# Kernel optimization log

Measured on AMD Instinct MI355X. Metric: run time of the kernel, lower is better.

The kernel has to match this reference:

```python
import jax, jax.numpy as jnp
import numpy as np

HIGH_THRESHOLD = 0.1
EPS = 1e-6


def _gaussian_kernel_2d(ksize=5, sigma=1.0):
    x = np.arange(ksize, dtype=np.float32) - ksize // 2
    g = np.exp(-(x * x) / (2.0 * sigma * sigma))
    g = g / g.sum()
    return (g[:, None] * g[None, :]).astype(np.float32)  # (5,5)


def _sobel_kernels():
    gx = np.array([[-1.0, 0.0, 1.0], [-2.0, 0.0, 2.0], [-1.0, 0.0, 1.0]], np.float32)
    gy = gx.T.copy()
    return np.stack([gx, gy])[:, None]  # (2,1,3,3)


def _nms_kernels():
    # kornia get_canny_nms_kernel: 8 direction kernels, center 1, -1 at neighbor
    k = np.zeros((8, 1, 3, 3), np.float32)
    k[:, 0, 1, 1] = 1.0
    offs = [(1, 2), (0, 2), (0, 1), (0, 0), (1, 0), (2, 0), (2, 1), (2, 2)]
    for i, (r, c) in enumerate(offs):
        k[i, 0, r, c] = -1.0
    return k


def _conv(x, w, pad, mode=None):
    # x: (B,Cin,H,W), w: (Cout,Cin,kh,kw)
    if mode is not None:
        x = jnp.pad(x, ((0, 0), (0, 0), (pad, pad), (pad, pad)), mode=mode)
        padding = 'VALID'
    else:
        padding = [(pad, pad), (pad, pad)]
    return jax.lax.conv_general_dilated(
        x, w, (1, 1), padding, dimension_numbers=('NCHW', 'OIHW', 'NCHW'))


def cal_edge(x):
    dt = x.dtype
    if x.shape[1] == 3:  # rgb_to_grayscale
        w = jnp.array([0.299, 0.587, 0.114], dt).reshape(1, 3, 1, 1)
        x = jnp.sum(x * w, axis=1, keepdims=True)
    # gaussian_blur2d, reflect border (kornia default)
    blurred = _conv(x, jnp.asarray(_gaussian_kernel_2d())[None, None], 2, mode='reflect')
    # spatial_gradient (sobel, replicate border)
    grads = _conv(blurred, jnp.asarray(_sobel_kernels()), 1, mode='edge')  # (B,2,H,W)
    gx, gy = grads[:, 0:1], grads[:, 1:2]
    magnitude = jnp.sqrt(gx * gx + gy * gy + EPS)  # (B,1,H,W)
    angle = jnp.arctan2(gy, gx) * (180.0 / np.pi)
    angle = jnp.round(angle / 45.0) * 45.0
    nms_mag = _conv(magnitude, jnp.asarray(_nms_kernels()), 1)  # (B,8,H,W), zero pad
    pos_idx = jnp.mod(angle / 45.0, 8.0).astype(jnp.int32)        # (B,1,H,W)
    neg_idx = jnp.mod(angle / 45.0 + 4.0, 8.0).astype(jnp.int32)
    cp = jnp.take_along_axis(nms_mag, pos_idx, axis=1)
    cn = jnp.take_along_axis(nms_mag, neg_idx, axis=1)
    is_max = jnp.minimum(cp, cn) > 0.0
    magnitude = magnitude * is_max
    # F.threshold(mag, high, 0); then F.threshold(-e, -high, -1); e = -e
    e1 = jnp.where(magnitude > HIGH_THRESHOLD, magnitude, jnp.zeros((), dt))
    edges = -jnp.where(-e1 > -HIGH_THRESHOLD, -e1, jnp.full((), -1.0, dt))
    return edges


def setup_inputs() -> dict:
    key = jax.random.key(0)
    k1, k2 = jax.random.split(key)
    shape = (8, 3, 1024, 1024)
    op = jax.random.uniform(k1, shape, jnp.float32)
    gt = jax.random.uniform(k2, shape, jnp.float32)
    return {'op': op, 'gt': gt}


def reference(op, gt):
    edge_op = cal_edge(op)
    edge_gt = cal_edge(gt)
    return jnp.mean(jnp.abs(edge_op - edge_gt))
```

## Files before the change

### kernel.cpp

```cpp
#include <hip/hip_runtime.h>

#define N 1024
#define NN (N * N)
#define STRIPS 19
#define SEGS 64
#define SEGROWS 16
#define NUNITS (STRIPS * SEGS * 8)

__device__ __forceinline__ int refl(int i) {
    if (i < 0) return -i;
    if (i >= N) return 2 * N - 2 - i;
    return i;
}

#define ROW_BODY(yv, DO_NMS)                                                      \
  {                                                                               \
    int rr = ROWE ? refl(yv) : (yv);                                              \
    const float* ra = A + (size_t)rr * N;      \
    const float* rb = B + (size_t)rr * N;                                         \
    float ga = 0.299f * ra[cR] + 0.587f * ra[cR + NN] + 0.114f * ra[cR + 2 * NN]; \
    float gb = 0.299f * rb[cR] + 0.587f * rb[cR + NN] + 0.114f * rb[cR + 2 * NN]; \
    float gal2 = __shfl(ga, iL2, 64), gal1 = __shfl(ga, iL1, 64);                 \
    float gar1 = __shfl(ga, iR1, 64), gar2 = __shfl(ga, iR2, 64);                 \
    float gbl2 = __shfl(gb, iL2, 64), gbl1 = __shfl(gb, iL1, 64);                 \
    float gbr1 = __shfl(gb, iR1, 64), gbr2 = __shfl(gb, iR2, 64);                 \
    float hna = w0*gal2 + w1*gal1 + w2*ga + w3*gar1 + w4*gar2;                    \
    float hnb = w0*gbl2 + w1*gbl1 + w2*gb + w3*gbr1 + w4*gbr2;                    \
    ha0=ha1; ha1=ha2; ha2=ha3; ha3=ha4; ha4=hna;                                  \
    hb0=hb1; hb1=hb2; hb2=hb3; hb3=hb4; hb4=hnb;                                  \
    float bna = w0*ha0 + w1*ha1 + w2*ha2 + w3*ha3 + w4*ha4;                       \
    float bnb = w0*hb0 + w1*hb1 + w2*hb2 + w3*hb3 + w4*hb4;                       \
    bla0=bla1; bla1=bla2; bla2=bna;                                               \
    blb0=blb1; blb1=blb2; blb2=bnb;                                               \
    float Ara, Cra, Arb, Crb;                                                     \
    if (ROWE) {                                                                   \
      int z = (yv) - 3;                                                           \
      Ara = (z == 0)     ? bla1 : bla0;                                           \
      Cra = (z == N - 1) ? bla1 : bla2;                                           \
      Arb = (z == 0)     ? blb1 : blb0;                                           \
      Crb = (z == N - 1) ? blb1 : blb2;                                           \
    } else { Ara = bla0; Cra = bla2; Arb = blb0; Crb = blb2; }                    \
    float sa = Ara + 2.f*bla1 + Cra;  float da = Cra - Ara;                       \
    float sb = Arb + 2.f*blb1 + Crb;  float db = Crb - Arb;                       \
    float sal = __shfl(sa, iL1, 64), sar = __shfl(sa, iR1, 64);                   \
    float dal = __shfl(da, iL1, 64), dar = __shfl(da, iR1, 64);                   \
    float sbl = __shfl(sb, iL1, 64), sbr = __shfl(sb, iR1, 64);                   \
    float dbl = __shfl(db, iL1, 64), dbr = __shfl(db, iR1, 64);                   \
    if (COLE) {                                                                   \
      sal = cz0 ? sa : sal;  dal = cz0 ? da : dal;                                \
      sar = czN ? sa : sar;  dar = czN ? da : dar;                                \
      sbl = cz0 ? sb : sbl;  dbl = cz0 ? db : dbl;                                \
      sbr = czN ? sb : sbr;  dbr = czN ? db : dbr;                                \
    }                                                                             \
    float gxa = sar - sal;            float gya = dal + 2.f*da + dar;             \
    float gxb = sbr - sbl;            float gyb = dbl + 2.f*db + dbr;             \
    float maga = sqrtf(gxa*gxa + gya*gya + 1e-6f);                                \
    float magb = sqrtf(gxb*gxb + gyb*gyb + 1e-6f);                                \
    float axx = fabsf(gxa), ayy = fabsf(gya);                                     \
    int cda = (ayy <= 0.41421356f * axx) ? 0                                      \
            : (ayy >= 2.41421356f * axx) ? 1                                      \
            : (((gxa > 0.f) == (gya > 0.f)) ? 2 : 3);                             \
    float bxx = fabsf(gxb), byy = fabsf(gyb);                                     \
    int cdb = (byy <= 0.41421356f * bxx) ? 0                                      \
            : (byy >= 2.41421356f * bxx) ? 1                                      \
            : (((gxb > 0.f) == (gyb > 0.f)) ? 2 : 3);                             \
    float mala = __shfl(maga, iL1, 64); if (COLE) mala = cz0 ? 0.f : mala;        \
    float mara = __shfl(maga, iR1, 64); if (COLE) mara = czN ? 0.f : mara;        \
    float malb = __shfl(magb, iL1, 64); if (COLE) malb = cz0 ? 0.f : malb;        \
    float marb = __shfl(magb, iR1, 64); if (COLE) marb = czN ? 0.f : marb;        \
    mga0=mga1;   mga1=mga2;   mga2=maga;                                          \
    mgla0=mgla1; mgla1=mgla2; mgla2=mala;                                         \
    mgra0=mgra1; mgra1=mgra2; mgra2=mara;                                         \
    mgb0=mgb1;   mgb1=mgb2;   mgb2=magb;                                          \
    mglb0=mglb1; mglb1=mglb2; mglb2=malb;                                         \
    mgrb0=mgrb1; mgrb1=mgrb2; mgrb2=marb;                                         \
    int axUa = axa; axa = cda;                                                    \
    int axUb = axb; axb = cdb;                                                    \
    if (DO_NMS) {                                                                 \
      float m0a = mga0, l0a = mgla0, r0a = mgra0;                                 \
      float m2a = mga2, l2a = mgla2, r2a = mgra2;                                 \
      float m0b = mgb0, l0b = mglb0, r0b = mgrb0;                                 \
      float m2b = mgb2, l2b = mglb2, r2b = mgrb2;                                 \
      if (ROWE) {                                                                 \
        int w = (yv) - 4;                                                         \
        if (w == 0)     { m0a=0; l0a=0; r0a=0; m0b=0; l0b=0; r0b=0; }             \
        if (w == N - 1) { m2a=0; l2a=0; r2a=0; m2b=0; l2b=0; r2b=0; }             \
      }                                                                           \
      float n1a = (axUa == 0) ? mgra1 : (axUa == 1) ? m0a : (axUa == 2) ? r0a : l0a; \
      float n2a = (axUa == 0) ? mgla1 : (axUa == 1) ? m2a : (axUa == 2) ? l2a : r2a; \
      float n1b = (axUb == 0) ? mgrb1 : (axUb == 1) ? m0b : (axUb == 2) ? r0b : l0b; \
      float n2b = (axUb == 0) ? mglb1 : (axUb == 1) ? m2b : (axUb == 2) ? l2b : r2b; \
      bool ea = (mga1 > n1a) && (mga1 > n2a) && (mga1 > 0.1f);                    \
      bool eb = (mgb1 > n1b) && (mgb1 > n2b) && (mgb1 > 0.1f);                    \
      acc += (int)(valid && (ea != eb));                                          \
    }                                                                             \
  }

template<bool COLE, bool ROWE>
__device__ __forceinline__ void edge_unit(
    const float* __restrict__ op, const float* __restrict__ gt,
    unsigned int* __restrict__ partials,
    int unit, int img, int strip, int seg, int lane)
{
    const float w0 = 0.05448868f, w1 = 0.24420134f, w2 = 0.40261996f,
                w3 = 0.24420134f, w4 = 0.05448868f;

    int cb = strip * 56 - 4;
    int c  = cb + lane;
    int cR = COLE ? refl(c) : c;

    const float* A = op + (size_t)img * 3 * NN;
    const float* B = gt + (size_t)img * 3 * NN;

    const bool cz0 = COLE && (c == 0);
    const bool czN = COLE && (c == N - 1);
    const bool valid = (lane >= 4) && (lane <= 59) &&
                       (!COLE || ((c >= 0) && (c < N)));

    const int iL1 = lane - 1, iL2 = lane - 2, iR1 = lane + 1, iR2 = lane + 2;

    float ha0=0,ha1=0,ha2=0,ha3=0,ha4=0;
    float bla0=0,bla1=0,bla2=0;
    float mga0=0,mga1=0,mga2=0;
    float mgla0=0,mgla1=0,mgla2=0;
    float mgra0=0,mgra1=0,mgra2=0;
    int   axa = 0;
    float hb0=0,hb1=0,hb2=0,hb3=0,hb4=0;
    float blb0=0,blb1=0,blb2=0;
    float mgb0=0,mgb1=0,mgb2=0;
    float mglb0=0,mglb1=0,mglb2=0;
    float mgrb0=0,mgrb1=0,mgrb2=0;
    int   axb = 0;

    int acc = 0;
    const int R0 = seg * SEGROWS;

#pragma unroll 4
    for (int y = R0 - 4; y < R0 + 4; ++y) ROW_BODY(y, 0)

#pragma unroll 4
    for (int y = R0 + 4; y <= R0 + SEGROWS + 3; ++y) ROW_BODY(y, 1)

    for (int off = 32; off > 0; off >>= 1)
        acc += __shfl_down(acc, off, 64);
    if (lane == 0)
        partials[unit] = (unsigned int)acc;
}

__global__ __launch_bounds__(256)
void edge_diff_kernel(const float* __restrict__ op, const float* __restrict__ gt,
                      unsigned int* __restrict__ partials)
{
    int lane = threadIdx.x & 63;
    int unit = blockIdx.x * 4 + (threadIdx.x >> 6);
    int img  = unit / (STRIPS * SEGS);
    int rem  = unit - img * (STRIPS * SEGS);
    int strip = rem >> 6;
    int seg   = rem & (SEGS - 1);

    bool cole = (strip == 0) || (strip == STRIPS - 1);
    bool rowe = (seg == 0)   || (seg == SEGS - 1);

    if (!cole) {
        if (!rowe) edge_unit<false, false>(op, gt, partials, unit, img, strip, seg, lane);
        else       edge_unit<false, true >(op, gt, partials, unit, img, strip, seg, lane);
    } else {
        if (!rowe) edge_unit<true,  false>(op, gt, partials, unit, img, strip, seg, lane);
        else       edge_unit<true,  true >(op, gt, partials, unit, img, strip, seg, lane);
    }
}

__global__ __launch_bounds__(256)
void finalize_kernel(const unsigned int* __restrict__ partials, float* __restrict__ out)
{
    __shared__ unsigned int ws[4];
    int tid = threadIdx.x;
    unsigned int sum = 0;
    for (int i = tid; i < NUNITS; i += 256)
        sum += partials[i];
    int d = (int)sum;
    for (int off = 32; off > 0; off >>= 1)
        d += __shfl_down(d, off, 64);
    if ((tid & 63) == 0) ws[tid >> 6] = (unsigned int)d;
    __syncthreads();
    if (tid == 0)
        out[0] = (float)(ws[0] + ws[1] + ws[2] + ws[3]) / 8388608.0f;
}

extern "C" void kernel_launch(void* const* d_in, const int* in_sizes, int n_in,
                              void* d_out, int out_size, void* d_ws, size_t ws_size,
                              hipStream_t stream)
{
    const float* op = (const float*)d_in[0];
    const float* gt = (const float*)d_in[1];
    unsigned int* partials = (unsigned int*)d_ws;

    edge_diff_kernel<<<dim3(NUNITS / 4), dim3(256), 0, stream>>>(op, gt, partials);
    finalize_kernel<<<1, dim3(256), 0, stream>>>(partials, (float*)d_out);
}
```

Measured before the change: 238.9 us.

## Process four columns per lane with float4 loads and register-prefetched rows

Each lane now handles four adjacent columns using float4 loads, so a wavefront covers 248 output columns instead of 56. This cuts the strip count from 19 to 5 and shrinks the halo redundancy and the number of cross-lane shuffles per pixel. Row data is prefetched two rows ahead into registers, and the non-maximum-suppression results are packed into bitmasks counted with popc. The row-edge warmup now runs the full pipeline stages. The cost is much higher register pressure from the four-wide state arrays, which may lower occupancy, and far fewer blocks are launched.

Result: slower. 360.6 us (+50.9%).

```diff
diff --git a/kernel.cpp b/kernel.cpp
--- a/kernel.cpp
+++ b/kernel.cpp
@@ -2,10 +2,11 @@
 
 #define N 1024
 #define NN (N * N)
-#define STRIPS 19
+#define STRIPS 5
 #define SEGS 64
 #define SEGROWS 16
 #define NUNITS (STRIPS * SEGS * 8)
+#define NBLOCKS (NUNITS / 4)
 
 __device__ __forceinline__ int refl(int i) {
     if (i < 0) return -i;
@@ -13,87 +14,139 @@
     return i;
 }
 
-#define ROW_BODY(yv, DO_NMS)                                                      \
-  {                                                                               \
-    int rr = ROWE ? refl(yv) : (yv);                                              \
-    const float* ra = A + (size_t)rr * N;      \
-    const float* rb = B + (size_t)rr * N;                                         \
-    float ga = 0.299f * ra[cR] + 0.587f * ra[cR + NN] + 0.114f * ra[cR + 2 * NN]; \
-    float gb = 0.299f * rb[cR] + 0.587f * rb[cR + NN] + 0.114f * rb[cR + 2 * NN]; \
-    float gal2 = __shfl(ga, iL2, 64), gal1 = __shfl(ga, iL1, 64);                 \
-    float gar1 = __shfl(ga, iR1, 64), gar2 = __shfl(ga, iR2, 64);                 \
-    float gbl2 = __shfl(gb, iL2, 64), gbl1 = __shfl(gb, iL1, 64);                 \
-    float gbr1 = __shfl(gb, iR1, 64), gbr2 = __shfl(gb, iR2, 64);                 \
-    float hna = w0*gal2 + w1*gal1 + w2*ga + w3*gar1 + w4*gar2;                    \
-    float hnb = w0*gbl2 + w1*gbl1 + w2*gb + w3*gbr1 + w4*gbr2;                    \
-    ha0=ha1; ha1=ha2; ha2=ha3; ha3=ha4; ha4=hna;                                  \
-    hb0=hb1; hb1=hb2; hb2=hb3; hb3=hb4; hb4=hnb;                                  \
-    float bna = w0*ha0 + w1*ha1 + w2*ha2 + w3*ha3 + w4*ha4;                       \
-    float bnb = w0*hb0 + w1*hb1 + w2*hb2 + w3*hb3 + w4*hb4;                       \
-    bla0=bla1; bla1=bla2; bla2=bna;                                               \
-    blb0=blb1; blb1=blb2; blb2=bnb;                                               \
-    float Ara, Cra, Arb, Crb;                                                     \
-    if (ROWE) {                                                                   \
-      int z = (yv) - 3;                                                           \
-      Ara = (z == 0)     ? bla1 : bla0;                                           \
-      Cra = (z == N - 1) ? bla1 : bla2;                                           \
-      Arb = (z == 0)     ? blb1 : blb0;                                           \
-      Crb = (z == N - 1) ? blb1 : blb2;                                           \
-    } else { Ara = bla0; Cra = bla2; Arb = blb0; Crb = blb2; }                    \
-    float sa = Ara + 2.f*bla1 + Cra;  float da = Cra - Ara;                       \
-    float sb = Arb + 2.f*blb1 + Crb;  float db = Crb - Arb;                       \
-    float sal = __shfl(sa, iL1, 64), sar = __shfl(sa, iR1, 64);                   \
-    float dal = __shfl(da, iL1, 64), dar = __shfl(da, iR1, 64);                   \
-    float sbl = __shfl(sb, iL1, 64), sbr = __shfl(sb, iR1, 64);                   \
-    float dbl = __shfl(db, iL1, 64), dbr = __shfl(db, iR1, 64);                   \
-    if (COLE) {                                                                   \
-      sal = cz0 ? sa : sal;  dal = cz0 ? da : dal;                                \
-      sar = czN ? sa : sar;  dar = czN ? da : dar;                                \
-      sbl = cz0 ? sb : sbl;  dbl = cz0 ? db : dbl;                                \
-      sbr = czN ? sb : sbr;  dbr = czN ? db : dbr;                                \
-    }                                                                             \
-    float gxa = sar - sal;            float gya = dal + 2.f*da + dar;             \
-    float gxb = sbr - sbl;            float gyb = dbl + 2.f*db + dbr;             \
-    float maga = sqrtf(gxa*gxa + gya*gya + 1e-6f);                                \
-    float magb = sqrtf(gxb*gxb + gyb*gyb + 1e-6f);                                \
-    float axx = fabsf(gxa), ayy = fabsf(gya);                                     \
-    int cda = (ayy <= 0.41421356f * axx) ? 0                                      \
-            : (ayy >= 2.41421356f * axx) ? 1                                      \
-            : (((gxa > 0.f) == (gya > 0.f)) ? 2 : 3);                             \
-    float bxx = fabsf(gxb), byy = fabsf(gyb);                                     \
-    int cdb = (byy <= 0.41421356f * bxx) ? 0                                      \
-            : (byy >= 2.41421356f * bxx) ? 1                                      \
-            : (((gxb > 0.f) == (gyb > 0.f)) ? 2 : 3);                             \
-    float mala = __shfl(maga, iL1, 64); if (COLE) mala = cz0 ? 0.f : mala;        \
-    float mara = __shfl(maga, iR1, 64); if (COLE) mara = czN ? 0.f : mara;        \
-    float malb = __shfl(magb, iL1, 64); if (COLE) malb = cz0 ? 0.f : malb;        \
-    float marb = __shfl(magb, iR1, 64); if (COLE) marb = czN ? 0.f : marb;        \
-    mga0=mga1;   mga1=mga2;   mga2=maga;                                          \
-    mgla0=mgla1; mgla1=mgla2; mgla2=mala;                                         \
-    mgra0=mgra1; mgra1=mgra2; mgra2=mara;                                         \
-    mgb0=mgb1;   mgb1=mgb2;   mgb2=magb;                                          \
-    mglb0=mglb1; mglb1=mglb2; mglb2=malb;                                         \
-    mgrb0=mgrb1; mgrb1=mgrb2; mgrb2=marb;                                         \
-    int axUa = axa; axa = cda;                                                    \
-    int axUb = axb; axb = cdb;                                                    \
-    if (DO_NMS) {                                                                 \
-      float m0a = mga0, l0a = mgla0, r0a = mgra0;                                 \
-      float m2a = mga2, l2a = mgla2, r2a = mgra2;                                 \
-      float m0b = mgb0, l0b = mglb0, r0b = mgrb0;                                 \
-      float m2b = mgb2, l2b = mglb2, r2b = mgrb2;                                 \
-      if (ROWE) {                                                                 \
-        int w = (yv) - 4;                                                         \
-        if (w == 0)     { m0a=0; l0a=0; r0a=0; m0b=0; l0b=0; r0b=0; }             \
-        if (w == N - 1) { m2a=0; l2a=0; r2a=0; m2b=0; l2b=0; r2b=0; }             \
-      }                                                                           \
-      float n1a = (axUa == 0) ? mgra1 : (axUa == 1) ? m0a : (axUa == 2) ? r0a : l0a; \
-      float n2a = (axUa == 0) ? mgla1 : (axUa == 1) ? m2a : (axUa == 2) ? l2a : r2a; \
-      float n1b = (axUb == 0) ? mgrb1 : (axUb == 1) ? m0b : (axUb == 2) ? r0b : l0b; \
-      float n2b = (axUb == 0) ? mglb1 : (axUb == 1) ? m2b : (axUb == 2) ? l2b : r2b; \
-      bool ea = (mga1 > n1a) && (mga1 > n2a) && (mga1 > 0.1f);                    \
-      bool eb = (mgb1 > n1b) && (mgb1 > n2b) && (mgb1 > 0.1f);                    \
-      acc += (int)(valid && (ea != eb));                                          \
-    }                                                                             \
+template<bool COLE, bool ROWE, int STAGE>
+static __device__ __forceinline__ int img_row(
+    int yv, float g0, float g1, float g2, float g3,
+    float (&h)[4][5], float (&bl)[4][3], float (&mg)[4][3],
+    float (&mL)[3], float (&mR)[3], int (&ax)[4], int (&axU)[4],
+    bool cz0, bool czN, int iL1, int iR1)
+{
+    const float w0 = 0.05448868f, w1 = 0.24420134f, w2 = 0.40261996f,
+                w3 = 0.24420134f, w4 = 0.05448868f;
+
+    float gm2 = __shfl(g2, iL1, 64), gm1 = __shfl(g3, iL1, 64);
+    float gp4 = __shfl(g0, iR1, 64), gp5 = __shfl(g1, iR1, 64);
+    float hn0 = w0*gm2 + w1*gm1 + w2*g0 + w3*g1 + w4*g2;
+    float hn1 = w0*gm1 + w1*g0 + w2*g1 + w3*g2 + w4*g3;
+    float hn2 = w0*g0  + w1*g1 + w2*g2 + w3*g3 + w4*gp4;
+    float hn3 = w0*g1  + w1*g2 + w2*g3 + w3*gp4 + w4*gp5;
+#pragma unroll
+    for (int j = 0; j < 4; ++j) {
+#pragma unroll
+        for (int k = 0; k < 4; ++k) h[j][k] = h[j][k+1];
+    }
+    h[0][4]=hn0; h[1][4]=hn1; h[2][4]=hn2; h[3][4]=hn3;
+    if (STAGE < 1) return 0;
+
+    float bn[4];
+#pragma unroll
+    for (int j = 0; j < 4; ++j)
+        bn[j] = w0*h[j][0] + w1*h[j][1] + w2*h[j][2] + w3*h[j][3] + w4*h[j][4];
+#pragma unroll
+    for (int j = 0; j < 4; ++j) { bl[j][0]=bl[j][1]; bl[j][1]=bl[j][2]; bl[j][2]=bn[j]; }
+    if (STAGE < 2) return 0;
+
+    float s[4], d[4];
+#pragma unroll
+    for (int j = 0; j < 4; ++j) {
+        float A_, C_;
+        if (ROWE) {
+            int z = yv - 3;
+            A_ = (z == 0)     ? bl[j][1] : bl[j][0];
+            C_ = (z == N - 1) ? bl[j][1] : bl[j][2];
+        } else { A_ = bl[j][0]; C_ = bl[j][2]; }
+        s[j] = A_ + 2.f*bl[j][1] + C_;
+        d[j] = C_ - A_;
+    }
+    float sL = __shfl(s[3], iL1, 64), dL = __shfl(d[3], iL1, 64);
+    float sR = __shfl(s[0], iR1, 64), dR = __shfl(d[0], iR1, 64);
+    if (COLE) {
+        sL = cz0 ? s[0] : sL;  dL = cz0 ? d[0] : dL;
+        sR = czN ? s[3] : sR;  dR = czN ? d[3] : dR;
+    }
+    float gx[4], gy[4];
+    gx[0] = s[1] - sL;   gy[0] = dL + 2.f*d[0] + d[1];
+    gx[1] = s[2] - s[0]; gy[1] = d[0] + 2.f*d[1] + d[2];
+    gx[2] = s[3] - s[1]; gy[2] = d[1] + 2.f*d[2] + d[3];
+    gx[3] = sR - s[2];   gy[3] = d[2] + 2.f*d[3] + dR;
+
+    float m[4]; int cd[4];
+#pragma unroll
+    for (int j = 0; j < 4; ++j) {
+        m[j] = sqrtf(gx[j]*gx[j] + gy[j]*gy[j] + 1e-6f);
+        float ax_ = fabsf(gx[j]), ay_ = fabsf(gy[j]);
+        cd[j] = (ay_ <= 0.41421356f * ax_) ? 0
+              : (ay_ >= 2.41421356f * ax_) ? 1
+              : (((gx[j] > 0.f) == (gy[j] > 0.f)) ? 2 : 3);
+    }
+    float mLn = __shfl(m[3], iL1, 64);
+    float mRn = __shfl(m[0], iR1, 64);
+    if (COLE) { mLn = cz0 ? 0.f : mLn;  mRn = czN ? 0.f : mRn; }
+#pragma unroll
+    for (int j = 0; j < 4; ++j) { mg[j][0]=mg[j][1]; mg[j][1]=mg[j][2]; mg[j][2]=m[j]; }
+    mL[0]=mL[1]; mL[1]=mL[2]; mL[2]=mLn;
+    mR[0]=mR[1]; mR[1]=mR[2]; mR[2]=mRn;
+#pragma unroll
+    for (int j = 0; j < 4; ++j) { axU[j] = ax[j]; ax[j] = cd[j]; }
+    if (STAGE < 3) return 0;
+
+    float rm1[6] = { mL[0], mg[0][0], mg[1][0], mg[2][0], mg[3][0], mR[0] };
+    float rc [6] = { mL[1], mg[0][1], mg[1][1], mg[2][1], mg[3][1], mR[1] };
+    float rp1[6] = { mL[2], mg[0][2], mg[1][2], mg[2][2], mg[3][2], mR[2] };
+    if (ROWE) {
+        int w = yv - 4;
+        if (w == 0) {
+#pragma unroll
+            for (int j = 0; j < 6; ++j) rm1[j] = 0.f;
+        }
+        if (w == N - 1) {
+#pragma unroll
+            for (int j = 0; j < 6; ++j) rp1[j] = 0.f;
+        }
+    }
+    int em = 0;
+#pragma unroll
+    for (int j = 1; j <= 4; ++j) {
+        int a_ = axU[j-1];
+        float n1 = (a_ == 0) ? rc[j+1] : (a_ == 1) ? rm1[j] : (a_ == 2) ? rm1[j+1] : rm1[j-1];
+        float n2 = (a_ == 0) ? rc[j-1] : (a_ == 1) ? rp1[j] : (a_ == 2) ? rp1[j-1] : rp1[j+1];
+        bool e = (rc[j] > n1) && (rc[j] > n2) && (rc[j] > 0.1f);
+        em |= (int)e << (j-1);
+    }
+    return em;
+}
+
+#define LOADROW(k, rrv) { size_t o_ = (size_t)(rrv) * N;                          \
+    if (!COLE) {                                                                  \
+      vAr##k = *(const float4*)(Ar + o_); vAg##k = *(const float4*)(Ag + o_);     \
+      vAb##k = *(const float4*)(Ab + o_);                                         \
+      vBr##k = *(const float4*)(Br + o_); vBg##k = *(const float4*)(Bg + o_);     \
+      vBb##k = *(const float4*)(Bb + o_);                                         \
+    } else {                                                                      \
+      vAr##k.x = Ar[o_+rq0]; vAr##k.y = Ar[o_+rq1]; vAr##k.z = Ar[o_+rq2]; vAr##k.w = Ar[o_+rq3]; \
+      vAg##k.x = Ag[o_+rq0]; vAg##k.y = Ag[o_+rq1]; vAg##k.z = Ag[o_+rq2]; vAg##k.w = Ag[o_+rq3]; \
+      vAb##k.x = Ab[o_+rq0]; vAb##k.y = Ab[o_+rq1]; vAb##k.z = Ab[o_+rq2]; vAb##k.w = Ab[o_+rq3]; \
+      vBr##k.x = Br[o_+rq0]; vBr##k.y = Br[o_+rq1]; vBr##k.z = Br[o_+rq2]; vBr##k.w = Br[o_+rq3]; \
+      vBg##k.x = Bg[o_+rq0]; vBg##k.y = Bg[o_+rq1]; vBg##k.z = Bg[o_+rq2]; vBg##k.w = Bg[o_+rq3]; \
+      vBb##k.x = Bb[o_+rq0]; vBb##k.y = Bb[o_+rq1]; vBb##k.z = Bb[o_+rq2]; vBb##k.w = Bb[o_+rq3]; \
+    } }
+
+#define BODY(yv, STAGE, kb, RELOAD) {                                             \
+    float ga0 = 0.299f*vAr##kb.x + 0.587f*vAg##kb.x + 0.114f*vAb##kb.x;           \
+    float ga1 = 0.299f*vAr##kb.y + 0.587f*vAg##kb.y + 0.114f*vAb##kb.y;           \
+    float ga2 = 0.299f*vAr##kb.z + 0.587f*vAg##kb.z + 0.114f*vAb##kb.z;           \
+    float ga3 = 0.299f*vAr##kb.w + 0.587f*vAg##kb.w + 0.114f*vAb##kb.w;           \
+    float gb0 = 0.299f*vBr##kb.x + 0.587f*vBg##kb.x + 0.114f*vBb##kb.x;           \
+    float gb1 = 0.299f*vBr##kb.y + 0.587f*vBg##kb.y + 0.114f*vBb##kb.y;           \
+    float gb2 = 0.299f*vBr##kb.z + 0.587f*vBg##kb.z + 0.114f*vBb##kb.z;           \
+    float gb3 = 0.299f*vBr##kb.w + 0.587f*vBg##kb.w + 0.114f*vBb##kb.w;           \
+    if (RELOAD) { int n_ = (yv) + 2; int r_ = ROWE ? refl(n_) : (n_);             \
+                  LOADROW(kb, r_) }                                               \
+    int emA = img_row<COLE,ROWE,STAGE>((yv), ga0,ga1,ga2,ga3,                     \
+                  ah,abl,amg,amL,amR,aax,aaxU, cz0,czN,iL1,iR1);                  \
+    int emB = img_row<COLE,ROWE,STAGE>((yv), gb0,gb1,gb2,gb3,                     \
+                  bh,bbl,bmg,bmL,bmR,bax,baxU, cz0,czN,iL1,iR1);                  \
+    if ((STAGE) >= 3) acc += valid ? __popc(emA ^ emB) : 0;                       \
   }
 
 template<bool COLE, bool ROWE>
@@ -102,44 +155,60 @@
     unsigned int* __restrict__ partials,
     int unit, int img, int strip, int seg, int lane)
 {
-    const float w0 = 0.05448868f, w1 = 0.24420134f, w2 = 0.40261996f,
-                w3 = 0.24420134f, w4 = 0.05448868f;
-
-    int cb = strip * 56 - 4;
-    int c  = cb + lane;
-    int cR = COLE ? refl(c) : c;
-
-    const float* A = op + (size_t)img * 3 * NN;
-    const float* B = gt + (size_t)img * 3 * NN;
-
-    const bool cz0 = COLE && (c == 0);
-    const bool czN = COLE && (c == N - 1);
-    const bool valid = (lane >= 4) && (lane <= 59) &&
-                       (!COLE || ((c >= 0) && (c < N)));
-
-    const int iL1 = lane - 1, iL2 = lane - 2, iR1 = lane + 1, iR2 = lane + 2;
-
-    float ha0=0,ha1=0,ha2=0,ha3=0,ha4=0;
-    float bla0=0,bla1=0,bla2=0;
-    float mga0=0,mga1=0,mga2=0;
-    float mgla0=0,mgla1=0,mgla2=0;
-    float mgra0=0,mgra1=0,mgra2=0;
-    int   axa = 0;
-    float hb0=0,hb1=0,hb2=0,hb3=0,hb4=0;
-    float blb0=0,blb1=0,blb2=0;
-    float mgb0=0,mgb1=0,mgb2=0;
-    float mglb0=0,mglb1=0,mglb2=0;
-    float mgrb0=0,mgrb1=0,mgrb2=0;
-    int   axb = 0;
+    const int cb = strip * 248 - 4;
+    const int c0 = cb + 4 * lane;
+
+    int rq0 = 0, rq1 = 0, rq2 = 0, rq3 = 0;
+    if (COLE) { rq0 = refl(c0); rq1 = refl(c0+1); rq2 = refl(c0+2); rq3 = refl(c0+3); }
+
+    const float* Ar = op + (size_t)img * 3 * NN + (COLE ? 0 : c0);
+    const float* Ag = Ar + NN;
+    const float* Ab = Ar + 2 * NN;
+    const float* Br = gt + (size_t)img * 3 * NN + (COLE ? 0 : c0);
+    const float* Bg = Br + NN;
+    const float* Bb = Br + 2 * NN;
+
+    const bool cz0 = COLE && (c0 == 0);
+    const bool czN = COLE && (c0 + 3 == N - 1);
+    const bool valid = (lane >= 1) && (lane <= 62) &&
+                       (!COLE || ((c0 >= 0) && (c0 + 3 < N)));
+
+    const int iL1 = lane - 1, iR1 = lane + 1;
+
+    float ah[4][5] = {}, bh[4][5] = {};
+    float abl[4][3] = {}, bbl[4][3] = {};
+    float amg[4][3] = {}, bmg[4][3] = {};
+    float amL[3] = {}, amR[3] = {}, bmL[3] = {}, bmR[3] = {};
+    int aax[4] = {}, aaxU[4] = {}, bax[4] = {}, baxU[4] = {};
+
+    float4 vAr0, vAg0, vAb0, vBr0, vBg0, vBb0;
+    float4 vAr1, vAg1, vAb1, vBr1, vBg1, vBb1;
 
     int acc = 0;
     const int R0 = seg * SEGROWS;
 
-#pragma unroll 4
-    for (int y = R0 - 4; y < R0 + 4; ++y) ROW_BODY(y, 0)
-
-#pragma unroll 4
-    for (int y = R0 + 4; y <= R0 + SEGROWS + 3; ++y) ROW_BODY(y, 1)
+    if (!ROWE) {
+        LOADROW(0, R0 - 4) LOADROW(1, R0 - 3)
+        BODY(R0 - 4, 0, 0, 1) BODY(R0 - 3, 0, 1, 1)
+        BODY(R0 - 2, 0, 0, 1) BODY(R0 - 1, 0, 1, 1)
+        BODY(R0,     1, 0, 1) BODY(R0 + 1, 1, 1, 1)
+        BODY(R0 + 2, 2, 0, 1) BODY(R0 + 3, 2, 1, 1)
+    } else {
+        LOADROW(0, refl(R0 - 4)) LOADROW(1, refl(R0 - 3))
+        BODY(R0 - 4, 2, 0, 1) BODY(R0 - 3, 2, 1, 1)
+        BODY(R0 - 2, 2, 0, 1) BODY(R0 - 1, 2, 1, 1)
+        BODY(R0,     2, 0, 1) BODY(R0 + 1, 2, 1, 1)
+        BODY(R0 + 2, 2, 0, 1) BODY(R0 + 3, 2, 1, 1)
+    }
+
+#pragma unroll 1
+    for (int t = 0; t < 7; ++t) {
+        int y = R0 + 4 + 2 * t;
+        BODY(y,     3, 0, 1)
+        BODY(y + 1, 3, 1, 1)
+    }
+    BODY(R0 + SEGROWS + 2, 3, 0, 0)
+    BODY(R0 + SEGROWS + 3, 3, 1, 0)
 
     for (int off = 32; off > 0; off >>= 1)
         acc += __shfl_down(acc, off, 64);
@@ -195,6 +264,6 @@
     const float* gt = (const float*)d_in[1];
     unsigned int* partials = (unsigned int*)d_ws;
 
-    edge_diff_kernel<<<dim3(NUNITS / 4), dim3(256), 0, stream>>>(op, gt, partials);
+    edge_diff_kernel<<<dim3(NBLOCKS), dim3(256), 0, stream>>>(op, gt, partials);
     finalize_kernel<<<1, dim3(256), 0, stream>>>(partials, (float*)d_out);
 }
```
